# Optimization experiments

Hardware: AMD Instinct MI355X
Metric: run time of the kernel (lower is better)

The kernel has to match this reference:

```python
import jax, jax.numpy as jnp
import numpy as np
import math

# SLAYER SRM-alpha neuron constants (theta=10, tauSr=tauRef=10, Ts=1, scaleRef=2)
THETA = 10.0
TAU = 10.0
A = math.exp(-1.0 / TAU)          # per-step decay of alpha kernel
B1 = math.e * A / TAU             # k[1] where k[t] = (t/tau)*exp(1 - t/tau), k[0]=0
REF_SCALE = 2.0 * THETA           # refractory kernel = -scaleRef*theta * alpha(t)
SG_ALPHA = 10.0                   # surrogate width = tauRho * theta


def psp(x):
    """Causal alpha-kernel (SRM) filter along last (time) axis.
    y[t] = sum_{tau<t} k[t-tau] x[tau], realized as 2nd-order IIR:
    y[t] = 2A y[t-1] - A^2 y[t-2] + B1 x[t-1].
    x: [..., T] -> [..., T]
    """
    xt = jnp.moveaxis(x, -1, 0)  # [T, ...]
    z = jnp.zeros_like(xt[0])

    def step(c, x_t):
        y1, y2, xp = c
        y = 2.0 * A * y1 - (A * A) * y2 + B1 * xp
        return (y, y1, x_t), y

    _, ys = jax.lax.scan(step, (z, z, z), xt)
    return jnp.moveaxis(ys, 0, -1)


def spike(u):
    """SLAYER spike generation with refractory feedback.
    At each step, membrane u is reduced by -2*theta*alpha-filtered past spikes,
    then thresholded at theta. u: [..., T] -> binary spikes [..., T].
    """
    ut = jnp.moveaxis(u, -1, 0)
    z = jnp.zeros_like(ut[0])

    def step(c, u_t):
        y1, y2, sp = c
        y = 2.0 * A * y1 - (A * A) * y2 + B1 * sp  # alpha response to past spikes
        s = (u_t - REF_SCALE * y >= THETA).astype(u_t.dtype)
        return (y, y1, s), s

    _, ss = jax.lax.scan(step, (z, z, z), ut)
    return jnp.moveaxis(ss, 0, -1)


def conv2d_t(x, w, pad):
    """Per-timestep 2D conv. x: [B,C,H,W,T], w: [O,I,kh,kw]."""
    B, C, H, W, T = x.shape
    xb = jnp.moveaxis(x, -1, 1).reshape(B * T, C, H, W)
    y = jax.lax.conv_general_dilated(
        xb, w, window_strides=(1, 1), padding=[(pad, pad), (pad, pad)],
        dimension_numbers=("NCHW", "OIHW", "NCHW"))
    O = w.shape[0]
    return jnp.moveaxis(y.reshape(B, T, O, H, W), 1, -1)


def pool2(x):
    """SLAYER sum-pool: fixed conv with all weights = 1.1*theta, stride 2."""
    y = jax.lax.reduce_window(x, 0.0, jax.lax.add,
                              (1, 1, 2, 2, 1), (1, 1, 2, 2, 1), "VALID")
    return y * (1.1 * THETA)


def dense_t(x, w):
    """x: [B,C,H,W,T] or [B,F,T]; w: [O,F]. Flattens (C,H,W) -> F."""
    B = x.shape[0]
    T = x.shape[-1]
    f = x.reshape(B, -1, T)
    return jnp.einsum("of,bft->bot", w, f)


def setup_inputs() -> dict:
    key = jax.random.key(0)
    ks = jax.random.split(key, 6)
    B, T = 4, 100
    s_in = (jax.random.uniform(ks[0], (B, 2, 128, 128, T)) < 0.05).astype(jnp.float32)

    def mkw(k, shape, ws):
        fan = float(np.prod(shape[1:]))
        return jax.random.normal(k, shape, jnp.float32) * (ws / math.sqrt(fan))

    w1 = mkw(ks[1], (32, 2, 5, 5), 10.0)      # SC1, weightScale=10
    w2 = mkw(ks[2], (64, 32, 3, 3), 20.0)     # SC2, weightScale=20
    w3 = mkw(ks[3], (128, 64, 3, 3), 20.0)    # SC3, weightScale=20
    wf4a = mkw(ks[4], (512, 128 * 8 * 8), 1.0)  # SF4a
    wf4b = mkw(ks[5], (11, 512), 1.0)           # SF4b
    return {"s_in": s_in, "w1": w1, "w2": w2, "w3": w3, "wf4a": wf4a, "wf4b": wf4b}


def reference(s_in, w1, w2, w3, wf4a, wf4b):
    x = spike(psp(pool2(s_in)))                 # SP0: [B,2,64,64,T]
    x = spike(psp(conv2d_t(x, w1, pad=2)))      # SC1: [B,32,64,64,T]
    x = spike(psp(pool2(x)))                    # SP1: [B,32,32,32,T]
    x = spike(psp(conv2d_t(x, w2, pad=1)))      # SC2: [B,64,32,32,T]
    x = spike(psp(pool2(x)))                    # SP2: [B,64,16,16,T]
    x = spike(psp(conv2d_t(x, w3, pad=1)))      # SC3: [B,128,16,16,T]
    x = spike(psp(pool2(x)))                    # SP3: [B,128,8,8,T]
    x = spike(psp(dense_t(x, wf4a)))            # SF4a: [B,512,T]
    # SD4 dropout: identity at inference
    x = spike(psp(dense_t(x, wf4b)))            # SF4b: [B,11,T]
    return x
```

## Files before the change

### kernel.cpp

```cpp
#include <hip/hip_runtime.h>

typedef unsigned long long ull;

__device__ constexpr float C1f = (float)1.80967483607191914632;
__device__ constexpr float C2f = (float)0.81873075307798185867;
__device__ constexpr float C3f = (float)0.24596031111569496638;

__device__ __forceinline__ float iir_spike_step(float acc, float& y1, float& y2, float& xp,
                                                float& r1, float& r2, float& sp) {
#pragma clang fp contract(off)
    float u = C1f * y1 - C2f * y2 + C3f * xp;
    float r = C1f * r1 - C2f * r2 + C3f * sp;
    float s = (u - 20.0f * r >= 10.0f) ? 1.0f : 0.0f;
    y2 = y1; y1 = u; xp = acc;
    r2 = r1; r1 = r; sp = s;
    return s;
}

template <int STRIDE>
__device__ __forceinline__ void sacc(float& acc, ull m, const float* __restrict__ ptr) {
    while (m) {
        ull m1 = m & (m - 1);
        ull m2 = m1 & (m1 - 1);
        ull m3 = m2 & (m2 - 1);
        if (m3) {
            int c0 = __builtin_ctzll(m);
            int c1 = __builtin_ctzll(m1);
            int c2 = __builtin_ctzll(m2);
            int c3 = __builtin_ctzll(m3);
            float w0 = ptr[c0 * STRIDE];
            float w1 = ptr[c1 * STRIDE];
            float w2 = ptr[c2 * STRIDE];
            float w3 = ptr[c3 * STRIDE];
            acc += w0; acc += w1; acc += w2; acc += w3;
            m = m3 & (m3 - 1);
        } else {
            acc += ptr[__builtin_ctzll(m) * STRIDE];
            m = m1;
        }
    }
}

__global__ void k_sp0(const float* __restrict__ s_in, ull* __restrict__ s0m) {
    int wid = (blockIdx.x * 256 + threadIdx.x) >> 6;
    int lane = threadIdx.x & 63;
    int h = wid & 63;
    int c = (wid >> 6) & 1;
    int b = wid >> 7;
    const float* p00 = s_in + ((size_t)(((b * 2 + c) * 128 + 2 * h) * 128 + 2 * lane)) * 100;
    const float* p01 = p00 + 100;
    const float* p10 = p00 + 12800;
    const float* p11 = p10 + 100;
    float y1 = 0, y2 = 0, xp = 0, r1 = 0, r2 = 0, sp = 0;
    for (int t = 0; t < 100; ++t) {
        float cnt = (p00[t] > 0.5f) + (p01[t] > 0.5f) + (p10[t] > 0.5f) + (p11[t] > 0.5f);
        float s = iir_spike_step(11.0f * cnt, y1, y2, xp, r1, r2, sp);
        ull m = __ballot(s > 0.5f);
        if (lane == 0) s0m[((size_t)(t * 4 + b) * 2 + c) * 64 + h] = m;
    }
}

__global__ void k_sc1(const ull* __restrict__ s0m, const float* __restrict__ w1,
                      ull* __restrict__ s1m) {
    int hg = blockIdx.x & 15;
    int o  = (blockIdx.x >> 4) & 31;
    int b  = blockIdx.x >> 9;
    float wr[50];
#pragma unroll
    for (int i = 0; i < 50; ++i) wr[i] = w1[o * 50 + i];
    int h = hg * 4 + (threadIdx.x >> 6);
    int lane = threadIdx.x & 63;
    int sh = lane - 2;
    float y1 = 0, y2 = 0, xp = 0, r1 = 0, r2 = 0, sp = 0;
    for (int t = 0; t < 100; ++t) {
        float acc = 0.0f;
        const ull* rb = s0m + (size_t)(t * 4 + b) * 128;
#pragma unroll
        for (int c = 0; c < 2; ++c) {
#pragma unroll
            for (int kh = 0; kh < 5; ++kh) {
                int ih = h - 2 + kh;
                ull m = (ih >= 0 && ih < 64) ? rb[c * 64 + ih] : 0ULL;
                unsigned pat = (sh >= 0) ? ((unsigned)(m >> sh) & 31u)
                                         : (((unsigned)m << (-sh)) & 31u);
#pragma unroll
                for (int j = 0; j < 5; ++j)
                    acc = fmaf((float)((pat >> j) & 1u), wr[c * 25 + kh * 5 + j], acc);
            }
        }
        float s = iir_spike_step(acc, y1, y2, xp, r1, r2, sp);
        ull mm = __ballot(s > 0.5f);
        if (lane == 0) s1m[((size_t)(t * 4 + b) * 32 + o) * 64 + h] = mm;
    }
}

__global__ void k_sp1(const ull* __restrict__ s1m, unsigned* __restrict__ s2m) {
    int wid = (blockIdx.x * 256 + threadIdx.x) >> 6;
    int lane = threadIdx.x & 63;
    int wop = wid & 15;
    int ho = (wid >> 4) & 31;
    int b = wid >> 9;
    int c = lane & 31;
    int q = lane >> 5;
    int w = wop * 2 + q;
    float y1 = 0, y2 = 0, xp = 0, r1 = 0, r2 = 0, sp = 0;
    for (int t = 0; t < 100; ++t) {
        const ull* base = s1m + ((size_t)(t * 4 + b) * 32 + c) * 64 + 2 * ho;
        ull m0 = base[0], m1 = base[1];
        unsigned v0 = (unsigned)(m0 >> (2 * w)) & 3u;
        unsigned v1 = (unsigned)(m1 >> (2 * w)) & 3u;
        float cnt = (float)((v0 & 1) + (v0 >> 1) + (v1 & 1) + (v1 >> 1));
        float s = iir_spike_step(11.0f * cnt, y1, y2, xp, r1, r2, sp);
        ull mm = __ballot(s > 0.5f);
        if (lane == 0)  s2m[((size_t)(t * 4 + b) * 32 + ho) * 32 + wop * 2]     = (unsigned)mm;
        if (lane == 32) s2m[((size_t)(t * 4 + b) * 32 + ho) * 32 + wop * 2 + 1] = (unsigned)(mm >> 32);
    }
}

__global__ void k_wT(const float* __restrict__ w2, const float* __restrict__ w3,
                     float* __restrict__ w2T, float* __restrict__ w3T) {
    int i = blockIdx.x * 256 + threadIdx.x;
    if (i < 9 * 32 * 64) {
        int o = i & 63; int c = (i >> 6) & 31; int p = i >> 11;
        w2T[i] = w2[(o * 32 + c) * 9 + p];
    }
    if (i < 9 * 64 * 128) {
        int o = i & 127; int c = (i >> 7) & 63; int p = i >> 13;
        w3T[i] = w3[(o * 64 + c) * 9 + p];
    }
}

__global__ void k_wT4a(const float* __restrict__ w, float* __restrict__ wT) {
    __shared__ float tile[64][65];
    int ft = blockIdx.x & 127;
    int ot = blockIdx.x >> 7;
    int j = threadIdx.x & 63;
    int i0 = threadIdx.x >> 6;
    for (int i = i0; i < 64; i += 4)
        tile[i][j] = w[(size_t)(ot * 64 + i) * 8192 + ft * 64 + j];
    __syncthreads();
    for (int i = i0; i < 64; i += 4)
        wT[(size_t)(ft * 64 + i) * 512 + ot * 64 + j] = tile[j][i];
}

__global__ __launch_bounds__(1024) void k_sc2(const unsigned* __restrict__ s2m,
                                              const float* __restrict__ w2T,
                                              ull* __restrict__ sc2m) {
    __shared__ float wl[4 * 32 * 64];
    for (int i = threadIdx.x; i < 4 * 32 * 64; i += 1024) wl[i] = w2T[i];
    __syncthreads();
    int task = blockIdx.x * 16 + (threadIdx.x >> 6);
    int pix = task & 1023;
    int b = task >> 10;
    int h = pix >> 5, w = pix & 31;
    int lane = threadIdx.x & 63;
    float y1 = 0, y2 = 0, xp = 0, r1 = 0, r2 = 0, sp = 0;
    for (int t = 0; t < 100; ++t) {
        const unsigned* mb = s2m + (size_t)(t * 4 + b) * 1024;
        float acc = 0.0f;
#pragma unroll
        for (int kh = 0; kh < 3; ++kh) {
            int ih = h - 1 + kh;
            if (ih < 0 || ih >= 32) continue;
#pragma unroll
            for (int kw = 0; kw < 3; ++kw) {
                int iw = w - 1 + kw;
                if (iw < 0 || iw >= 32) continue;
                unsigned m = __builtin_amdgcn_readfirstlane(mb[ih * 32 + iw]);
                int pos = kh * 3 + kw;
                if (pos < 4) sacc<64>(acc, (ull)m, wl  + pos * 2048 + lane);
                else         sacc<64>(acc, (ull)m, w2T + pos * 2048 + lane);
            }
        }
        float s = iir_spike_step(acc, y1, y2, xp, r1, r2, sp);
        ull mm = __ballot(s > 0.5f);
        if (lane == 0) sc2m[(size_t)(t * 4 + b) * 1024 + pix] = mm;
    }
}

__global__ void k_sp2(const ull* __restrict__ sc2m, ull* __restrict__ s3m) {
    int wid = (blockIdx.x * 256 + threadIdx.x) >> 6;
    int lane = threadIdx.x & 63;
    int wo = wid & 15;
    int ho = (wid >> 4) & 15;
    int b = wid >> 8;
    float y1 = 0, y2 = 0, xp = 0, r1 = 0, r2 = 0, sp = 0;
    for (int t = 0; t < 100; ++t) {
        const ull* mb = sc2m + (size_t)(t * 4 + b) * 1024 + (2 * ho) * 32 + 2 * wo;
        ull a0 = mb[0], a1 = mb[1], a2 = mb[32], a3 = mb[33];
        float cnt = (float)(((a0 >> lane) & 1) + ((a1 >> lane) & 1) +
                            ((a2 >> lane) & 1) + ((a3 >> lane) & 1));
        float s = iir_spike_step(11.0f * cnt, y1, y2, xp, r1, r2, sp);
        ull mm = __ballot(s > 0.5f);
        if (lane == 0) s3m[(size_t)(t * 4 + b) * 256 + ho * 16 + wo] = mm;
    }
}

__global__ __launch_bounds__(512) void k_sc3(const ull* __restrict__ s3m,
                                             const float* __restrict__ w3T,
                                             ull* __restrict__ s4m) {
    __shared__ float wl[4 * 64 * 64];
    int half = blockIdx.x & 1;
    int rest = blockIdx.x >> 1;
    int pg = rest & 31;
    int b = rest >> 5;
    for (int i = threadIdx.x; i < 4 * 64 * 64; i += 512) {
        int o = i & 63; int pc = i >> 6;
        wl[i] = w3T[pc * 128 + half * 64 + o];
    }
    __syncthreads();
    int pix = pg * 8 + (threadIdx.x >> 6);
    int h = pix >> 4, w = pix & 15;
    int lane = threadIdx.x & 63;
    const float* wg = w3T + half * 64 + lane;
    float y1 = 0, y2 = 0, xp = 0, r1 = 0, r2 = 0, sp = 0;
    for (int t = 0; t < 100; ++t) {
        const ull* mb = s3m + (size_t)(t * 4 + b) * 256;
        float acc = 0.0f;
#pragma unroll
        for (int kh = 0; kh < 3; ++kh) {
            int ih = h - 1 + kh;
            if (ih < 0 || ih >= 16) continue;
#pragma unroll
            for (int kw = 0; kw < 3; ++kw) {
                int iw = w - 1 + kw;
                if (iw < 0 || iw >= 16) continue;
                ull mm64 = mb[ih * 16 + iw];
                unsigned lo = __builtin_amdgcn_readfirstlane((unsigned)mm64);
                unsigned hi = __builtin_amdgcn_readfirstlane((unsigned)(mm64 >> 32));
                ull m = ((ull)hi << 32) | lo;
                int pos = kh * 3 + kw;
                if (pos < 4) sacc<64>(acc, m, wl + pos * 4096 + lane);
                else         sacc<128>(acc, m, wg + pos * 64 * 128);
            }
        }
        float s = iir_spike_step(acc, y1, y2, xp, r1, r2, sp);
        ull mm = __ballot(s > 0.5f);
        if (lane == 0) s4m[((size_t)(t * 4 + b) * 256 + pix) * 2 + half] = mm;
    }
}

__global__ void k_sp3(const ull* __restrict__ s4m, ull* __restrict__ s5m) {
    int wid = (blockIdx.x * 256 + threadIdx.x) >> 6;
    int lane = threadIdx.x & 63;
    int c = wid & 127;
    int b = wid >> 7;
    int half = c >> 6;
    int cbit = c & 63;
    int ho = lane >> 3, wo = lane & 7;
    float y1 = 0, y2 = 0, xp = 0, r1 = 0, r2 = 0, sp = 0;
    for (int t = 0; t < 100; ++t) {
        const ull* mb = s4m + ((size_t)(t * 4 + b) * 256 + (2 * ho) * 16 + 2 * wo) * 2 + half;
        ull a0 = mb[0], a1 = mb[2], a2 = mb[32], a3 = mb[34];
        float cnt = (float)(((a0 >> cbit) & 1) + ((a1 >> cbit) & 1) +
                            ((a2 >> cbit) & 1) + ((a3 >> cbit) & 1));
        float s = iir_spike_step(11.0f * cnt, y1, y2, xp, r1, r2, sp);
        ull mm = __ballot(s > 0.5f);
        if (lane == 0) s5m[(size_t)(t * 4 + b) * 128 + c] = mm;
    }
}

__global__ void k_gemm4a(const ull* __restrict__ s5m,
                         const float* __restrict__ wT,
                         float* __restrict__ acc_out) {
    int wg = blockIdx.x * 4 + (threadIdx.x >> 6);
    int lane = threadIdx.x & 63;
    int ot = wg & 7;
    int tb = wg >> 3;
    const ull* mp = s5m + (size_t)tb * 128;
    const float* wbase = wT + ot * 64 + lane;
    float acc = 0.0f;
    for (int c = 0; c < 128; ++c) {
        ull mv = mp[c];
        unsigned lo = __builtin_amdgcn_readfirstlane((unsigned)mv);
        unsigned hi = __builtin_amdgcn_readfirstlane((unsigned)(mv >> 32));
        ull m = ((ull)hi << 32) | lo;
        sacc<512>(acc, m, wbase + (size_t)(c * 64) * 512);
    }
    acc_out[(size_t)tb * 512 + ot * 64 + lane] = acc;
}

__global__ void k_iir4a(const float* __restrict__ accbuf, unsigned char* __restrict__ s6) {
    int id = blockIdx.x * 64 + threadIdx.x;
    int b = id >> 9, o = id & 511;
    float y1 = 0, y2 = 0, xp = 0, r1 = 0, r2 = 0, sp = 0;
    for (int t = 0; t < 100; ++t) {
        float a = accbuf[(size_t)(t * 4 + b) * 512 + o];
        float s = iir_spike_step(a, y1, y2, xp, r1, r2, sp);
        s6[(size_t)(t * 4 + b) * 512 + o] = (unsigned char)s;
    }
}

__global__ void k_dense4b(const unsigned char* __restrict__ in,
                          const float* __restrict__ wt,
                          float* __restrict__ out) {
    int wid = blockIdx.x;
    int lane = threadIdx.x;
    int o = wid % 11;
    int b = wid / 11;
    float wreg[8];
    const float* wp = wt + o * 512 + lane * 8;
#pragma unroll
    for (int k = 0; k < 8; ++k) wreg[k] = wp[k];
    float y1 = 0, y2 = 0, xp = 0, r1 = 0, r2 = 0, sp = 0;
    for (int t = 0; t < 100; ++t) {
        const unsigned char* ip = in + (size_t)(t * 4 + b) * 512 + lane * 8;
        uchar4 a = *(const uchar4*)ip;
        uchar4 c = *(const uchar4*)(ip + 4);
        float acc = wreg[0] * (float)a.x + wreg[1] * (float)a.y +
                    wreg[2] * (float)a.z + wreg[3] * (float)a.w +
                    wreg[4] * (float)c.x + wreg[5] * (float)c.y +
                    wreg[6] * (float)c.z + wreg[7] * (float)c.w;
#pragma unroll
        for (int off = 32; off > 0; off >>= 1) acc += __shfl_xor(acc, off, 64);
        float s = iir_spike_step(acc, y1, y2, xp, r1, r2, sp);
        if (lane == 0) out[(b * 11 + o) * 100 + t] = s;
    }
}

extern "C" void kernel_launch(void* const* d_in, const int* in_sizes, int n_in,
                              void* d_out, int out_size, void* d_ws, size_t ws_size,
                              hipStream_t stream) {
    const float* s_in = (const float*)d_in[0];
    const float* w1   = (const float*)d_in[1];
    const float* w2   = (const float*)d_in[2];
    const float* w3   = (const float*)d_in[3];
    const float* w4a  = (const float*)d_in[4];
    const float* w4b  = (const float*)d_in[5];
    float* out = (float*)d_out;

    char* ws = (char*)d_ws;
    ull*           s0m  = (ull*)(ws + 0);
    ull*           s1m  = (ull*)(ws + 409600);
    unsigned*      s2m  = (unsigned*)(ws + 6963200);
    ull*           sc2m = (ull*)(ws + 8601600);
    ull*           s3m  = (ull*)(ws + 11878400);
    ull*           s4m  = (ull*)(ws + 12697600);
    ull*           s5m  = (ull*)(ws + 14336000);
    unsigned char* s6   = (unsigned char*)(ws + 14745600);
    float*         accA = (float*)(ws + 14950400);
    float*         w2T  = (float*)(ws + 15769600);
    float*         w3T  = (float*)(ws + 15843328);
    float*         wT4a = (float*)(ws + 16138240);

    k_wT<<<288, 256, 0, stream>>>(w2, w3, w2T, w3T);
    k_wT4a<<<1024, 256, 0, stream>>>(w4a, wT4a);
    k_sp0<<<128, 256, 0, stream>>>(s_in, s0m);
    k_sc1<<<2048, 256, 0, stream>>>(s0m, w1, s1m);
    k_sp1<<<512, 256, 0, stream>>>(s1m, s2m);
    k_sc2<<<256, 1024, 0, stream>>>(s2m, w2T, sc2m);
    k_sp2<<<256, 256, 0, stream>>>(sc2m, s3m);
    k_sc3<<<256, 512, 0, stream>>>(s3m, w3T, s4m);
    k_sp3<<<128, 256, 0, stream>>>(s4m, s5m);
    k_gemm4a<<<800, 256, 0, stream>>>(s5m, wT4a, accA);
    k_iir4a<<<32, 64, 0, stream>>>(accA, s6);
    k_dense4b<<<44, 64, 0, stream>>>(s6, w4b, out);
}
```

Baseline: 1.581 ms.

## Stage full conv weights in LDS, unroll popcount accumulation by eight, transpose SC1 output

Stages all nine 3x3 weight positions for SC2 and SC3 in dynamic shared memory, where before only four were staged and the rest came from global memory. This removes the global-load path for the remaining positions. The sparse bit-mask accumulation loop now handles eight set bits per iteration to expose more independent loads. The SC1 spike-mask layout is transposed so SP1 reads adjacent rows more contiguously. The larger LDS footprint (72KB and 144KB) may cut blocks per CU, and the 144KB request for SC3 may exceed the LDS available per workgroup on this target.

Result: no change. 1.597 ms (+1.0%).

```diff
diff --git a/kernel.cpp b/kernel.cpp
--- a/kernel.cpp
+++ b/kernel.cpp
@@ -23,17 +23,29 @@
         ull m1 = m & (m - 1);
         ull m2 = m1 & (m1 - 1);
         ull m3 = m2 & (m2 - 1);
-        if (m3) {
-            int c0 = __builtin_ctzll(m);
-            int c1 = __builtin_ctzll(m1);
-            int c2 = __builtin_ctzll(m2);
-            int c3 = __builtin_ctzll(m3);
-            float w0 = ptr[c0 * STRIDE];
-            float w1 = ptr[c1 * STRIDE];
-            float w2 = ptr[c2 * STRIDE];
-            float w3 = ptr[c3 * STRIDE];
+        ull m4 = m3 & (m3 - 1);
+        ull m5 = m4 & (m4 - 1);
+        ull m6 = m5 & (m5 - 1);
+        ull m7 = m6 & (m6 - 1);
+        if (m7) {
+            float w0 = ptr[__builtin_ctzll(m)  * STRIDE];
+            float w1 = ptr[__builtin_ctzll(m1) * STRIDE];
+            float w2 = ptr[__builtin_ctzll(m2) * STRIDE];
+            float w3 = ptr[__builtin_ctzll(m3) * STRIDE];
+            float w4 = ptr[__builtin_ctzll(m4) * STRIDE];
+            float w5 = ptr[__builtin_ctzll(m5) * STRIDE];
+            float w6 = ptr[__builtin_ctzll(m6) * STRIDE];
+            float w7 = ptr[__builtin_ctzll(m7) * STRIDE];
             acc += w0; acc += w1; acc += w2; acc += w3;
-            m = m3 & (m3 - 1);
+            acc += w4; acc += w5; acc += w6; acc += w7;
+            m = m7 & (m7 - 1);
+        } else if (m3) {
+            float w0 = ptr[__builtin_ctzll(m)  * STRIDE];
+            float w1 = ptr[__builtin_ctzll(m1) * STRIDE];
+            float w2 = ptr[__builtin_ctzll(m2) * STRIDE];
+            float w3 = ptr[__builtin_ctzll(m3) * STRIDE];
+            acc += w0; acc += w1; acc += w2; acc += w3;
+            m = m4;
         } else {
             acc += ptr[__builtin_ctzll(m) * STRIDE];
             m = m1;
@@ -90,7 +102,7 @@
         }
         float s = iir_spike_step(acc, y1, y2, xp, r1, r2, sp);
         ull mm = __ballot(s > 0.5f);
-        if (lane == 0) s1m[((size_t)(t * 4 + b) * 32 + o) * 64 + h] = mm;
+        if (lane == 0) s1m[((size_t)(t * 4 + b) * 64 + h) * 32 + o] = mm;
     }
 }
 
@@ -105,8 +117,8 @@
     int w = wop * 2 + q;
     float y1 = 0, y2 = 0, xp = 0, r1 = 0, r2 = 0, sp = 0;
     for (int t = 0; t < 100; ++t) {
-        const ull* base = s1m + ((size_t)(t * 4 + b) * 32 + c) * 64 + 2 * ho;
-        ull m0 = base[0], m1 = base[1];
+        const ull* base = s1m + ((size_t)(t * 4 + b) * 64 + 2 * ho) * 32 + c;
+        ull m0 = base[0], m1 = base[32];
         unsigned v0 = (unsigned)(m0 >> (2 * w)) & 3u;
         unsigned v1 = (unsigned)(m1 >> (2 * w)) & 3u;
         float cnt = (float)((v0 & 1) + (v0 >> 1) + (v1 & 1) + (v1 >> 1));
@@ -146,8 +158,8 @@
 __global__ __launch_bounds__(1024) void k_sc2(const unsigned* __restrict__ s2m,
                                               const float* __restrict__ w2T,
                                               ull* __restrict__ sc2m) {
-    __shared__ float wl[4 * 32 * 64];
-    for (int i = threadIdx.x; i < 4 * 32 * 64; i += 1024) wl[i] = w2T[i];
+    extern __shared__ float wl[];
+    for (int i = threadIdx.x; i < 9 * 32 * 64; i += 1024) wl[i] = w2T[i];
     __syncthreads();
     int task = blockIdx.x * 16 + (threadIdx.x >> 6);
     int pix = task & 1023;
@@ -167,9 +179,7 @@
                 int iw = w - 1 + kw;
                 if (iw < 0 || iw >= 32) continue;
                 unsigned m = __builtin_amdgcn_readfirstlane(mb[ih * 32 + iw]);
-                int pos = kh * 3 + kw;
-                if (pos < 4) sacc<64>(acc, (ull)m, wl  + pos * 2048 + lane);
-                else         sacc<64>(acc, (ull)m, w2T + pos * 2048 + lane);
+                sacc<64>(acc, (ull)m, wl + (kh * 3 + kw) * 2048 + lane);
             }
         }
         float s = iir_spike_step(acc, y1, y2, xp, r1, r2, sp);
@@ -199,12 +209,12 @@
 __global__ __launch_bounds__(512) void k_sc3(const ull* __restrict__ s3m,
                                              const float* __restrict__ w3T,
                                              ull* __restrict__ s4m) {
-    __shared__ float wl[4 * 64 * 64];
+    extern __shared__ float wl[];
     int half = blockIdx.x & 1;
     int rest = blockIdx.x >> 1;
     int pg = rest & 31;
     int b = rest >> 5;
-    for (int i = threadIdx.x; i < 4 * 64 * 64; i += 512) {
+    for (int i = threadIdx.x; i < 9 * 64 * 64; i += 512) {
         int o = i & 63; int pc = i >> 6;
         wl[i] = w3T[pc * 128 + half * 64 + o];
     }
@@ -212,7 +222,6 @@
     int pix = pg * 8 + (threadIdx.x >> 6);
     int h = pix >> 4, w = pix & 15;
     int lane = threadIdx.x & 63;
-    const float* wg = w3T + half * 64 + lane;
     float y1 = 0, y2 = 0, xp = 0, r1 = 0, r2 = 0, sp = 0;
     for (int t = 0; t < 100; ++t) {
         const ull* mb = s3m + (size_t)(t * 4 + b) * 256;
@@ -229,9 +238,7 @@
                 unsigned lo = __builtin_amdgcn_readfirstlane((unsigned)mm64);
                 unsigned hi = __builtin_amdgcn_readfirstlane((unsigned)(mm64 >> 32));
                 ull m = ((ull)hi << 32) | lo;
-                int pos = kh * 3 + kw;
-                if (pos < 4) sacc<64>(acc, m, wl + pos * 4096 + lane);
-                else         sacc<128>(acc, m, wg + pos * 64 * 128);
+                sacc<64>(acc, m, wl + (kh * 3 + kw) * 4096 + lane);
             }
         }
         float s = iir_spike_step(acc, y1, y2, xp, r1, r2, sp);
@@ -343,14 +350,17 @@
     float*         w3T  = (float*)(ws + 15843328);
     float*         wT4a = (float*)(ws + 16138240);
 
+    hipFuncSetAttribute((const void*)k_sc2, hipFuncAttributeMaxDynamicSharedMemorySize, 73728);
+    hipFuncSetAttribute((const void*)k_sc3, hipFuncAttributeMaxDynamicSharedMemorySize, 147456);
+
     k_wT<<<288, 256, 0, stream>>>(w2, w3, w2T, w3T);
     k_wT4a<<<1024, 256, 0, stream>>>(w4a, wT4a);
     k_sp0<<<128, 256, 0, stream>>>(s_in, s0m);
     k_sc1<<<2048, 256, 0, stream>>>(s0m, w1, s1m);
     k_sp1<<<512, 256, 0, stream>>>(s1m, s2m);
-    k_sc2<<<256, 1024, 0, stream>>>(s2m, w2T, sc2m);
+    k_sc2<<<256, 1024, 73728, stream>>>(s2m, w2T, sc2m);
     k_sp2<<<256, 256, 0, stream>>>(sc2m, s3m);
-    k_sc3<<<256, 512, 0, stream>>>(s3m, w3T, s4m);
+    k_sc3<<<256, 512, 147456, stream>>>(s3m, w3T, s4m);
     k_sp3<<<128, 256, 0, stream>>>(s4m, s5m);
     k_gemm4a<<<800, 256, 0, stream>>>(s5m, wT4a, accA);
     k_iir4a<<<32, 64, 0, stream>>>(accA, s6);
```

## Stage full conv weights in LDS, process two timesteps per iteration, transpose s1m layout

Applied to the files above, without the earlier changes.

The sc2 and sc3 convolution kernels now copy all nine kernel positions of the weights into dynamic LDS, where before four came from LDS and five from global memory. They also process two timesteps per loop iteration with a branchless paired sparse-accumulate that pads empty slots with a zero LDS entry, which adds memory-level parallelism to the gathers. The SC1 output layout moves channel to the innermost index so the SP1 reads are coalesced across lanes. The trade-offs are much larger LDS use per block (about 145 KB for sc3), which lowers occupancy, and wasted zero loads when the two timesteps have uneven spike counts.

After: 1.424 ms. -9.9%, faster.

```diff
diff --git a/kernel.cpp b/kernel.cpp
--- a/kernel.cpp
+++ b/kernel.cpp
@@ -41,6 +41,25 @@
     }
 }
 
+__device__ __forceinline__ void sacc2(float& a0, ull m0, float& a1, ull m1,
+                                      const float* __restrict__ wl,
+                                      int posoff, int zoff, int lane) {
+    while (m0 | m1) {
+        int i00 = m0 ? posoff + (int)__builtin_ctzll(m0) * 64 + lane : zoff + lane; m0 &= m0 - 1;
+        int i01 = m0 ? posoff + (int)__builtin_ctzll(m0) * 64 + lane : zoff + lane; m0 &= m0 - 1;
+        int i02 = m0 ? posoff + (int)__builtin_ctzll(m0) * 64 + lane : zoff + lane; m0 &= m0 - 1;
+        int i03 = m0 ? posoff + (int)__builtin_ctzll(m0) * 64 + lane : zoff + lane; m0 &= m0 - 1;
+        int i10 = m1 ? posoff + (int)__builtin_ctzll(m1) * 64 + lane : zoff + lane; m1 &= m1 - 1;
+        int i11 = m1 ? posoff + (int)__builtin_ctzll(m1) * 64 + lane : zoff + lane; m1 &= m1 - 1;
+        int i12 = m1 ? posoff + (int)__builtin_ctzll(m1) * 64 + lane : zoff + lane; m1 &= m1 - 1;
+        int i13 = m1 ? posoff + (int)__builtin_ctzll(m1) * 64 + lane : zoff + lane; m1 &= m1 - 1;
+        float v00 = wl[i00], v01 = wl[i01], v02 = wl[i02], v03 = wl[i03];
+        float v10 = wl[i10], v11 = wl[i11], v12 = wl[i12], v13 = wl[i13];
+        a0 += v00; a0 += v01; a0 += v02; a0 += v03;
+        a1 += v10; a1 += v11; a1 += v12; a1 += v13;
+    }
+}
+
 __global__ void k_sp0(const float* __restrict__ s_in, ull* __restrict__ s0m) {
     int wid = (blockIdx.x * 256 + threadIdx.x) >> 6;
     int lane = threadIdx.x & 63;
@@ -90,7 +109,7 @@
         }
         float s = iir_spike_step(acc, y1, y2, xp, r1, r2, sp);
         ull mm = __ballot(s > 0.5f);
-        if (lane == 0) s1m[((size_t)(t * 4 + b) * 32 + o) * 64 + h] = mm;
+        if (lane == 0) s1m[((size_t)(t * 4 + b) * 64 + h) * 32 + o] = mm;
     }
 }
 
@@ -105,8 +124,8 @@
     int w = wop * 2 + q;
     float y1 = 0, y2 = 0, xp = 0, r1 = 0, r2 = 0, sp = 0;
     for (int t = 0; t < 100; ++t) {
-        const ull* base = s1m + ((size_t)(t * 4 + b) * 32 + c) * 64 + 2 * ho;
-        ull m0 = base[0], m1 = base[1];
+        const ull* base = s1m + ((size_t)(t * 4 + b) * 64 + 2 * ho) * 32 + c;
+        ull m0 = base[0], m1 = base[32];
         unsigned v0 = (unsigned)(m0 >> (2 * w)) & 3u;
         unsigned v1 = (unsigned)(m1 >> (2 * w)) & 3u;
         float cnt = (float)((v0 & 1) + (v0 >> 1) + (v1 & 1) + (v1 >> 1));
@@ -146,8 +165,10 @@
 __global__ __launch_bounds__(1024) void k_sc2(const unsigned* __restrict__ s2m,
                                               const float* __restrict__ w2T,
                                               ull* __restrict__ sc2m) {
-    __shared__ float wl[4 * 32 * 64];
-    for (int i = threadIdx.x; i < 4 * 32 * 64; i += 1024) wl[i] = w2T[i];
+    extern __shared__ float wl[];
+    const int ZOFF = 9 * 32 * 64;
+    for (int i = threadIdx.x; i < ZOFF; i += 1024) wl[i] = w2T[i];
+    if (threadIdx.x < 64) wl[ZOFF + threadIdx.x] = 0.0f;
     __syncthreads();
     int task = blockIdx.x * 16 + (threadIdx.x >> 6);
     int pix = task & 1023;
@@ -155,9 +176,10 @@
     int h = pix >> 5, w = pix & 31;
     int lane = threadIdx.x & 63;
     float y1 = 0, y2 = 0, xp = 0, r1 = 0, r2 = 0, sp = 0;
-    for (int t = 0; t < 100; ++t) {
-        const unsigned* mb = s2m + (size_t)(t * 4 + b) * 1024;
-        float acc = 0.0f;
+    for (int t = 0; t < 100; t += 2) {
+        const unsigned* mbA = s2m + (size_t)(t * 4 + b) * 1024;
+        const unsigned* mbB = mbA + 4096;
+        float acc0 = 0.0f, acc1 = 0.0f;
 #pragma unroll
         for (int kh = 0; kh < 3; ++kh) {
             int ih = h - 1 + kh;
@@ -166,15 +188,17 @@
             for (int kw = 0; kw < 3; ++kw) {
                 int iw = w - 1 + kw;
                 if (iw < 0 || iw >= 32) continue;
-                unsigned m = __builtin_amdgcn_readfirstlane(mb[ih * 32 + iw]);
-                int pos = kh * 3 + kw;
-                if (pos < 4) sacc<64>(acc, (ull)m, wl  + pos * 2048 + lane);
-                else         sacc<64>(acc, (ull)m, w2T + pos * 2048 + lane);
+                unsigned mA = __builtin_amdgcn_readfirstlane(mbA[ih * 32 + iw]);
+                unsigned mB = __builtin_amdgcn_readfirstlane(mbB[ih * 32 + iw]);
+                sacc2(acc0, (ull)mA, acc1, (ull)mB, wl, (kh * 3 + kw) * 2048, ZOFF, lane);
             }
         }
-        float s = iir_spike_step(acc, y1, y2, xp, r1, r2, sp);
-        ull mm = __ballot(s > 0.5f);
-        if (lane == 0) sc2m[(size_t)(t * 4 + b) * 1024 + pix] = mm;
+        float s0 = iir_spike_step(acc0, y1, y2, xp, r1, r2, sp);
+        ull mm0 = __ballot(s0 > 0.5f);
+        if (lane == 0) sc2m[(size_t)(t * 4 + b) * 1024 + pix] = mm0;
+        float s1 = iir_spike_step(acc1, y1, y2, xp, r1, r2, sp);
+        ull mm1 = __ballot(s1 > 0.5f);
+        if (lane == 0) sc2m[(size_t)((t + 1) * 4 + b) * 1024 + pix] = mm1;
     }
 }
 
@@ -199,24 +223,26 @@
 __global__ __launch_bounds__(512) void k_sc3(const ull* __restrict__ s3m,
                                              const float* __restrict__ w3T,
                                              ull* __restrict__ s4m) {
-    __shared__ float wl[4 * 64 * 64];
+    extern __shared__ float wl[];
+    const int ZOFF = 9 * 64 * 64;
     int half = blockIdx.x & 1;
     int rest = blockIdx.x >> 1;
     int pg = rest & 31;
     int b = rest >> 5;
-    for (int i = threadIdx.x; i < 4 * 64 * 64; i += 512) {
+    for (int i = threadIdx.x; i < ZOFF; i += 512) {
         int o = i & 63; int pc = i >> 6;
         wl[i] = w3T[pc * 128 + half * 64 + o];
     }
+    if (threadIdx.x < 64) wl[ZOFF + threadIdx.x] = 0.0f;
     __syncthreads();
     int pix = pg * 8 + (threadIdx.x >> 6);
     int h = pix >> 4, w = pix & 15;
     int lane = threadIdx.x & 63;
-    const float* wg = w3T + half * 64 + lane;
-    float y1 = 0, y2 = 0, xp = 0, r1 = 0, r2 = 0, sp = 0;
-    for (int t = 0; t < 100; ++t) {
-        const ull* mb = s3m + (size_t)(t * 4 + b) * 256;
-        float acc = 0.0f;
+    float y1 = 0, y2 = 0, xp = 0, r1 = 0, r2 = 0, sp = 0;
+    for (int t = 0; t < 100; t += 2) {
+        const ull* mbA = s3m + (size_t)(t * 4 + b) * 256;
+        const ull* mbB = mbA + 1024;
+        float acc0 = 0.0f, acc1 = 0.0f;
 #pragma unroll
         for (int kh = 0; kh < 3; ++kh) {
             int ih = h - 1 + kh;
@@ -225,18 +251,23 @@
             for (int kw = 0; kw < 3; ++kw) {
                 int iw = w - 1 + kw;
                 if (iw < 0 || iw >= 16) continue;
-                ull mm64 = mb[ih * 16 + iw];
-                unsigned lo = __builtin_amdgcn_readfirstlane((unsigned)mm64);
-                unsigned hi = __builtin_amdgcn_readfirstlane((unsigned)(mm64 >> 32));
-                ull m = ((ull)hi << 32) | lo;
-                int pos = kh * 3 + kw;
-                if (pos < 4) sacc<64>(acc, m, wl + pos * 4096 + lane);
-                else         sacc<128>(acc, m, wg + pos * 64 * 128);
+                ull mA64 = mbA[ih * 16 + iw];
+                ull mB64 = mbB[ih * 16 + iw];
+                unsigned loA = __builtin_amdgcn_readfirstlane((unsigned)mA64);
+                unsigned hiA = __builtin_amdgcn_readfirstlane((unsigned)(mA64 >> 32));
+                unsigned loB = __builtin_amdgcn_readfirstlane((unsigned)mB64);
+                unsigned hiB = __builtin_amdgcn_readfirstlane((unsigned)(mB64 >> 32));
+                ull mA = ((ull)hiA << 32) | loA;
+                ull mB = ((ull)hiB << 32) | loB;
+                sacc2(acc0, mA, acc1, mB, wl, (kh * 3 + kw) * 4096, ZOFF, lane);
             }
         }
-        float s = iir_spike_step(acc, y1, y2, xp, r1, r2, sp);
-        ull mm = __ballot(s > 0.5f);
-        if (lane == 0) s4m[((size_t)(t * 4 + b) * 256 + pix) * 2 + half] = mm;
+        float s0 = iir_spike_step(acc0, y1, y2, xp, r1, r2, sp);
+        ull mm0 = __ballot(s0 > 0.5f);
+        if (lane == 0) s4m[((size_t)(t * 4 + b) * 256 + pix) * 2 + half] = mm0;
+        float s1 = iir_spike_step(acc1, y1, y2, xp, r1, r2, sp);
+        ull mm1 = __ballot(s1 > 0.5f);
+        if (lane == 0) s4m[((size_t)((t + 1) * 4 + b) * 256 + pix) * 2 + half] = mm1;
     }
 }
 
@@ -343,14 +374,17 @@
     float*         w3T  = (float*)(ws + 15843328);
     float*         wT4a = (float*)(ws + 16138240);
 
+    hipFuncSetAttribute((const void*)k_sc2, hipFuncAttributeMaxDynamicSharedMemorySize, 73984);
+    hipFuncSetAttribute((const void*)k_sc3, hipFuncAttributeMaxDynamicSharedMemorySize, 147712);
+
     k_wT<<<288, 256, 0, stream>>>(w2, w3, w2T, w3T);
     k_wT4a<<<1024, 256, 0, stream>>>(w4a, wT4a);
     k_sp0<<<128, 256, 0, stream>>>(s_in, s0m);
     k_sc1<<<2048, 256, 0, stream>>>(s0m, w1, s1m);
     k_sp1<<<512, 256, 0, stream>>>(s1m, s2m);
-    k_sc2<<<256, 1024, 0, stream>>>(s2m, w2T, sc2m);
+    k_sc2<<<256, 1024, 73984, stream>>>(s2m, w2T, sc2m);
     k_sp2<<<256, 256, 0, stream>>>(sc2m, s3m);
-    k_sc3<<<256, 512, 0, stream>>>(s3m, w3T, s4m);
+    k_sc3<<<256, 512, 147712, stream>>>(s3m, w3T, s4m);
     k_sp3<<<128, 256, 0, stream>>>(s4m, s5m);
     k_gemm4a<<<800, 256, 0, stream>>>(s5m, wT4a, accA);
     k_iir4a<<<32, 64, 0, stream>>>(accA, s6);
```
